# Kernel optimization log

Hardware: AMD Instinct MI355X
Metric: run time of the kernel (lower is better)

## Reference

```python
import jax, jax.numpy as jnp
import numpy as np
from jax import lax

KERNEL = 31
SMOOTH = 0.001
PAD = KERNEL // 2


def _avg_pool2d(x):
    # torch F.avg_pool2d(kernel=31, stride=1, padding=15, count_include_pad=True):
    # sum over 31x31 window with zero padding, then divide by 31*31 always.
    s = lax.reduce_window(
        x, 0.0, lax.add,
        window_dimensions=(1, 1, KERNEL, KERNEL),
        window_strides=(1, 1, 1, 1),
        padding=((0, 0), (0, 0), (PAD, PAD), (PAD, PAD)),
    )
    return s / (KERNEL * KERNEL)


def setup_inputs() -> dict:
    key = jax.random.key(0)
    k1, k2 = jax.random.split(key)
    B, C, H, W = 32, 1, 1024, 1024
    output = jax.random.normal(k1, (B, C, H, W), dtype=jnp.float32)
    target = jax.random.uniform(k2, (B, C, H, W), dtype=jnp.float32)
    return {"output": output, "target": target}


def reference(output, target):
    out = jax.nn.sigmoid(output)
    weight = 1.0 + 5.0 * jnp.abs(_avg_pool2d(target) - target)  # [B,C,H,W]
    inter = jnp.sum(out * target * weight, axis=(2, 3)).reshape(-1, 1)      # [B*C,1]
    mask_sum = jnp.sum((target + out) * weight, axis=(2, 3)).reshape(-1, 1)  # [B*C,1]
    loss = 1.0 - (2.0 * inter + SMOOTH) / (mask_sum + SMOOTH)
    return jnp.mean(loss)
```

## Files before the change

### kernel.cpp

```cpp
#include <hip/hip_runtime.h>
#include <math.h>


namespace {
constexpr int Bn = 32;
constexpr int Hn = 1024;
constexpr int Wn = 1024;
constexpr int Rn = 15;
constexpr int TX = 256;
constexpr int YS = 128;
constexpr int NB = YS / 8;
constexpr int NCOL = TX + 32;
constexpr int PHYSW = (NCOL / 8) * 12;
constexpr float INV_KK = 1.0f / 961.0f;
}

__device__ __forceinline__ int phys(int i) { return i + ((i >> 3) << 2); }

__device__ __forceinline__ float ldcol(const float* p, int y, int col, bool xok) {
    return (xok && (unsigned)y < (unsigned)Hn) ? p[(size_t)y * Wn + col] : 0.0f;
}

__global__ __launch_bounds__(256, 4)
void dice_main(const float* __restrict__ logits, const float* __restrict__ tgt,
               float* __restrict__ acc)
{
    __shared__ __align__(16) float vbuf[8 * PHYSW];
    __shared__ float red[8];

    const int bid = blockIdx.x;
    const int b   = bid >> 5;
    const int rem = bid & 31;
    const int x0  = (rem >> 3) * TX;
    const int y0  = (rem & 7) * YS;
    const int t   = threadIdx.x;

    const float* tb = tgt    + (size_t)b * Hn * Wn;
    const float* ob = logits + (size_t)b * Hn * Wn;

    const int  col0 = x0 - Rn + t;
    const bool has2 = (t < 32);
    const int  col1 = col0 + 256;
    const bool xok0 = (col0 >= 0) && (col0 < Wn);
    const bool xok1 = (col1 >= 0) && (col1 < Wn);
    const int  pt   = phys(t);
    const int  pt2  = phys(256 + t);

    const int rr = t >> 5;
    const int jj = t & 31;
    const int xb = x0 + (jj << 3);

    float vs0 = 0.0f, vs1 = 0.0f;
    for (int yy = y0 - Rn; yy <= y0 + Rn; ++yy) {
        vs0 += ldcol(tb, yy, col0, xok0);
        if (has2) vs1 += ldcol(tb, yy, col1, xok1);
    }

    float pA[8], qA[8];
    #pragma unroll
    for (int r = 0; r < 8; ++r) {
        pA[r] = ldcol(tb, y0 + r + Rn, col0, xok0);
        qA[r] = has2 ? ldcol(tb, y0 + r + Rn, col1, xok1) : 0.0f;
    }
    float4 ct0, ct1, co0, co1;
    {
        const float* tp = tb + (size_t)(y0 + rr) * Wn + xb;
        const float* op = ob + (size_t)(y0 + rr) * Wn + xb;
        ct0 = ((const float4*)tp)[0]; ct1 = ((const float4*)tp)[1];
        co0 = ((const float4*)op)[0]; co1 = ((const float4*)op)[1];
    }

    float acc_i = 0.0f, acc_m = 0.0f;

    for (int it = 0; it < NB; ++it) {
        const int ya = y0 + it * 8;

        #pragma unroll
        for (int r = 0; r < 8; ++r) {
            const int yr = ya + r;
            if (it > 0 || r > 0) {
                vs0 += pA[r] - ldcol(tb, yr - Rn - 1, col0, xok0);
                if (has2) vs1 += qA[r] - ldcol(tb, yr - Rn - 1, col1, xok1);
            }
            vbuf[r * PHYSW + pt] = vs0;
            if (has2) vbuf[r * PHYSW + pt2] = vs1;
        }
        __syncthreads();

        float4 nt0, nt1, no0, no1;
        if (it + 1 < NB) {
            #pragma unroll
            for (int r = 0; r < 8; ++r) {
                pA[r] = ldcol(tb, ya + 8 + r + Rn, col0, xok0);
                if (has2) qA[r] = ldcol(tb, ya + 8 + r + Rn, col1, xok1);
            }
            const float* tp = tb + (size_t)(ya + 8 + rr) * Wn + xb;
            const float* op = ob + (size_t)(ya + 8 + rr) * Wn + xb;
            nt0 = ((const float4*)tp)[0]; nt1 = ((const float4*)tp)[1];
            no0 = ((const float4*)op)[0]; no1 = ((const float4*)op)[1];
        }

        {
            const float* vrow = &vbuf[rr * PHYSW];
            float w[40];
            #pragma unroll
            for (int k = 0; k < 10; ++k) {
                const float4 q = *(const float4*)&vrow[phys((jj << 3) + (k << 2))];
                w[4 * k + 0] = q.x; w[4 * k + 1] = q.y;
                w[4 * k + 2] = q.z; w[4 * k + 3] = q.w;
            }

            const float tc[8] = {ct0.x, ct0.y, ct0.z, ct0.w, ct1.x, ct1.y, ct1.z, ct1.w};
            const float oc[8] = {co0.x, co0.y, co0.z, co0.w, co1.x, co1.y, co1.z, co1.w};

            float s0 = 0.0f, s1 = 0.0f, s2 = 0.0f, s3 = 0.0f;
            #pragma unroll
            for (int c = 0; c < 28; c += 4) {
                s0 += w[c]; s1 += w[c + 1]; s2 += w[c + 2]; s3 += w[c + 3];
            }
            float s = (s0 + s1) + (s2 + s3) + w[28] + w[29] + w[30];
            #pragma unroll
            for (int m = 0; m < 8; ++m) {
                if (m > 0) s += w[30 + m] - w[m - 1];
                const float avg = s * INV_KK;
                const float wt  = 1.0f + 5.0f * fabsf(avg - tc[m]);
                const float sg  = 1.0f / (1.0f + __expf(-oc[m]));
                acc_i += sg * tc[m] * wt;
                acc_m += (tc[m] + sg) * wt;
            }
        }

        if (it + 1 < NB) { ct0 = nt0; ct1 = nt1; co0 = no0; co1 = no1; }
        __syncthreads();
    }

    #pragma unroll
    for (int off = 32; off > 0; off >>= 1) {
        acc_i += __shfl_down(acc_i, off);
        acc_m += __shfl_down(acc_m, off);
    }
    const int lane = t & 63;
    const int wv   = t >> 6;
    if (lane == 0) { red[wv * 2] = acc_i; red[wv * 2 + 1] = acc_m; }
    __syncthreads();
    if (t == 0) {
        atomicAdd(&acc[2 * b],     red[0] + red[2] + red[4] + red[6]);
        atomicAdd(&acc[2 * b + 1], red[1] + red[3] + red[5] + red[7]);
    }
}

__global__ void dice_final(const float* __restrict__ acc, float* __restrict__ out)
{
    const int t = threadIdx.x;
    float l = 0.0f;
    if (t < Bn) {
        const float I = acc[2 * t];
        const float M = acc[2 * t + 1];
        l = 1.0f - (2.0f * I + 0.001f) / (M + 0.001f);
    }
    #pragma unroll
    for (int off = 32; off > 0; off >>= 1) l += __shfl_down(l, off);
    if (t == 0) out[0] = l * (1.0f / 32.0f);
}

extern "C" void kernel_launch(void* const* d_in, const int* in_sizes, int n_in,
                              void* d_out, int out_size, void* d_ws, size_t ws_size,
                              hipStream_t stream)
{
    const float* logits = (const float*)d_in[0];
    const float* target = (const float*)d_in[1];
    float* acc = (float*)d_ws;

    hipMemsetAsync(d_ws, 0, 64 * sizeof(float), stream);
    dice_main<<<dim3(Bn * 32), dim3(256), 0, stream>>>(logits, target, acc);
    dice_final<<<dim3(1), dim3(64), 0, stream>>>(acc, (float*)d_out);
}
```

Baseline: 314.8 us.

## Double-buffer LDS column sums and prefetch subtracted rows with single barrier

Makes the shared column-sum buffer double-buffered so the trailing barrier per iteration can be dropped, leaving one barrier per row block. It also prefetches the rows leaving the vertical window into registers one iteration ahead, alongside the entering rows, so the global loads overlap with compute instead of stalling the update. A custom barrier waits only on LDS counters, not on pending global loads. The cost is twice the LDS footprint and more live registers, which may reduce occupancy.

```diff
diff --git a/kernel.cpp b/kernel.cpp
--- a/kernel.cpp
+++ b/kernel.cpp
@@ -21,11 +21,17 @@
     return (xok && (unsigned)y < (unsigned)Hn) ? p[(size_t)y * Wn + col] : 0.0f;
 }
 
+__device__ __forceinline__ void lds_barrier() {
+    asm volatile("s_waitcnt lgkmcnt(0)" ::: "memory");
+    __builtin_amdgcn_s_barrier();
+    asm volatile("" ::: "memory");
+}
+
 __global__ __launch_bounds__(256, 4)
 void dice_main(const float* __restrict__ logits, const float* __restrict__ tgt,
                float* __restrict__ acc)
 {
-    __shared__ __align__(16) float vbuf[8 * PHYSW];
+    __shared__ __align__(16) float vbuf[2][8 * PHYSW];
     __shared__ float red[8];
 
     const int bid = blockIdx.x;
@@ -56,11 +62,13 @@
         if (has2) vs1 += ldcol(tb, yy, col1, xok1);
     }
 
-    float pA[8], qA[8];
+    float pA[8], qA[8], sA[8], qS[8];
     #pragma unroll
     for (int r = 0; r < 8; ++r) {
         pA[r] = ldcol(tb, y0 + r + Rn, col0, xok0);
+        sA[r] = ldcol(tb, y0 + r - Rn - 1, col0, xok0);
         qA[r] = has2 ? ldcol(tb, y0 + r + Rn, col1, xok1) : 0.0f;
+        qS[r] = has2 ? ldcol(tb, y0 + r - Rn - 1, col1, xok1) : 0.0f;
     }
     float4 ct0, ct1, co0, co1;
     {
@@ -74,25 +82,30 @@
 
     for (int it = 0; it < NB; ++it) {
         const int ya = y0 + it * 8;
+        float* vb = vbuf[it & 1];
 
         #pragma unroll
         for (int r = 0; r < 8; ++r) {
-            const int yr = ya + r;
             if (it > 0 || r > 0) {
-                vs0 += pA[r] - ldcol(tb, yr - Rn - 1, col0, xok0);
-                if (has2) vs1 += qA[r] - ldcol(tb, yr - Rn - 1, col1, xok1);
+                vs0 += pA[r] - sA[r];
+                if (has2) vs1 += qA[r] - qS[r];
             }
-            vbuf[r * PHYSW + pt] = vs0;
-            if (has2) vbuf[r * PHYSW + pt2] = vs1;
+            vb[r * PHYSW + pt] = vs0;
+            if (has2) vb[r * PHYSW + pt2] = vs1;
         }
-        __syncthreads();
+
+        lds_barrier();
 
         float4 nt0, nt1, no0, no1;
         if (it + 1 < NB) {
             #pragma unroll
             for (int r = 0; r < 8; ++r) {
                 pA[r] = ldcol(tb, ya + 8 + r + Rn, col0, xok0);
-                if (has2) qA[r] = ldcol(tb, ya + 8 + r + Rn, col1, xok1);
+                sA[r] = ldcol(tb, ya + 8 + r - Rn - 1, col0, xok0);
+                if (has2) {
+                    qA[r] = ldcol(tb, ya + 8 + r + Rn, col1, xok1);
+                    qS[r] = ldcol(tb, ya + 8 + r - Rn - 1, col1, xok1);
+                }
             }
             const float* tp = tb + (size_t)(ya + 8 + rr) * Wn + xb;
             const float* op = ob + (size_t)(ya + 8 + rr) * Wn + xb;
@@ -101,7 +114,7 @@
         }
 
         {
-            const float* vrow = &vbuf[rr * PHYSW];
+            const float* vrow = &vb[rr * PHYSW];
             float w[40];
             #pragma unroll
             for (int k = 0; k < 10; ++k) {
@@ -131,7 +144,6 @@
         }
 
         if (it + 1 < NB) { ct0 = nt0; ct1 = nt1; co0 = no0; co1 = no1; }
-        __syncthreads();
     }
 
     #pragma unroll
```

Result: slower. 395.1 us (+25.5%).
